# Kernel optimization log

Measured on AMD Instinct MI355X. Metric: run time of the kernel, lower is better.

Reference implementation:

```python
import jax, jax.numpy as jnp
import numpy as np


def setup_inputs() -> dict:
    key = jax.random.key(0)
    kq, kk, kv = jax.random.split(key, 3)
    B, S, D = 4, 4096, 64
    return {
        "q": jax.random.normal(kq, (B, S, D), dtype=jnp.float32),
        "k": jax.random.normal(kk, (B, S, D), dtype=jnp.float32),
        "v": jax.random.normal(kv, (B, S, D), dtype=jnp.float32),
    }


def reference(q, k, v):
    B, S, D = q.shape
    scale = 1.0 / jnp.sqrt(jnp.asarray(D, dtype=q.dtype))
    # (B, S, S) full score matrix, as in the naive torch implementation
    scores = jnp.einsum("bqd,bkd->bqk", q, k) * scale
    causal_mask = jnp.tril(jnp.ones((S, S), dtype=bool))  # True = keep
    scores = jnp.where(causal_mask, scores, -jnp.inf)
    attn = jax.nn.softmax(scores, axis=-1)
    return jnp.einsum("bqk,bkd->bqd", attn, v)
```

## Files before the change

### kernel.cpp

```cpp
#include <hip/hip_runtime.h>
#include <hip/hip_bf16.h>

typedef __bf16 bf16x8 __attribute__((ext_vector_type(8)));
typedef __bf16 bf16x4 __attribute__((ext_vector_type(4)));
typedef float  floatx4 __attribute__((ext_vector_type(4)));

#define SD 4096
#define DH 64
#define NB 4

__device__ __forceinline__ float exp2fast(float x) { return __builtin_amdgcn_exp2f(x); }

__device__ __forceinline__ unsigned pack_bf16_2(float a, float b) {
    union { __bf16 h[2]; unsigned u; } cvt;
    cvt.h[0] = (__bf16)a; cvt.h[1] = (__bf16)b;
    return cvt.u;
}

__device__ __forceinline__ void sync_all() {
    asm volatile("s_waitcnt vmcnt(0) lgkmcnt(0)\n\ts_barrier" ::: "memory");
}

__device__ __forceinline__ void load_lds16(const void* g, void* l) {
    __builtin_amdgcn_global_load_lds(
        (const __attribute__((address_space(1))) unsigned int*)g,
        (__attribute__((address_space(3))) unsigned int*)l, 16, 0, 0);
}

__device__ __forceinline__ int swz8(int g) {
    int row = g >> 3, ch = g & 7;
    return row * 64 + ((ch ^ (row & 7)) << 3);
}

__global__ __launch_bounds__(256) void prep_kernel(const float* __restrict__ k,
                                                   const float* __restrict__ v,
                                                   __bf16* __restrict__ kbs,
                                                   __bf16* __restrict__ vts) {
    __shared__ __bf16 tile[64][72];
    const int bid = blockIdx.x;
    const int tid = threadIdx.x;
    const long base = (long)bid * 4096;

    {
        const float* src = k + base + tid * 16;
        float4 f0 = *(const float4*)(src);
        float4 f1 = *(const float4*)(src + 4);
        float4 f2 = *(const float4*)(src + 8);
        float4 f3 = *(const float4*)(src + 12);
        bf16x8 c0, c1;
        c0[0]=(__bf16)f0.x; c0[1]=(__bf16)f0.y; c0[2]=(__bf16)f0.z; c0[3]=(__bf16)f0.w;
        c0[4]=(__bf16)f1.x; c0[5]=(__bf16)f1.y; c0[6]=(__bf16)f1.z; c0[7]=(__bf16)f1.w;
        c1[0]=(__bf16)f2.x; c1[1]=(__bf16)f2.y; c1[2]=(__bf16)f2.z; c1[3]=(__bf16)f2.w;
        c1[4]=(__bf16)f3.x; c1[5]=(__bf16)f3.y; c1[6]=(__bf16)f3.z; c1[7]=(__bf16)f3.w;
        __bf16* dst = kbs + base;
        *(bf16x8*)(dst + swz8(tid * 2))     = c0;
        *(bf16x8*)(dst + swz8(tid * 2 + 1)) = c1;
    }
    {
        int r = tid >> 2, ds0 = (tid & 3) * 16;
#pragma unroll
        for (int i = 0; i < 4; ++i) {
            float4 f = *(const float4*)(v + base + r * 64 + ds0 + i * 4);
            tile[ds0 + i*4 + 0][r] = (__bf16)f.x;
            tile[ds0 + i*4 + 1][r] = (__bf16)f.y;
            tile[ds0 + i*4 + 2][r] = (__bf16)f.z;
            tile[ds0 + i*4 + 3][r] = (__bf16)f.w;
        }
    }
    __syncthreads();
    {
        __bf16* dst = vts + base;
#pragma unroll
        for (int h = 0; h < 2; ++h) {
            int qc = tid * 2 + h;
            int d = qc >> 3, c8 = (qc & 7) * 8;
            bf16x8 o;
#pragma unroll
            for (int i = 0; i < 8; ++i) {
                int col = c8 + i;
                int key = ((col >> 5) * 2 + ((col >> 2) & 1)) * 16
                        + ((col >> 3) & 3) * 4 + (col & 3);
                o[i] = tile[d][key];
            }
            *(bf16x8*)(dst + swz8(qc)) = o;
        }
    }
}

__global__ __launch_bounds__(256, 4) void fa_kernel(const float* __restrict__ q,
                                                    const __bf16* __restrict__ kbs,
                                                    const __bf16* __restrict__ vts,
                                                    __bf16* __restrict__ opart,
                                                    float* __restrict__ lpart) {
    __shared__ __bf16 smem[2][8192];

    const int tid  = threadIdx.x;
    const int wave = tid >> 6;
    const int lane = tid & 63;
    const int c    = lane & 15;
    const int quad = lane >> 4;
    const int bid   = blockIdx.x;
    const int batch = bid & 3;
    const int pr    = (bid >> 2) & 31;
    const int qr    = bid >> 7;
    const float sc = 0.125f * 1.4426950408889634f;

    const long offB = (long)batch * SD * DH;

    const int sw   = c & 7;
    const int off0 = ((quad ^ sw) << 3);
    const int off1 = (((quad + 4) ^ sw) << 3);
    const int rowc = c * 64;

    const long tileB = (long)batch * 64;

    auto stage = [&](int kt, int bufi) {
        const char* gsrc = (wave < 2)
            ? (const char*)(kbs + (tileB + kt) * 4096) + wave * 4096
            : (const char*)(vts + (tileB + kt) * 4096) + (wave - 2) * 4096;
        char* ldst = (char*)(&smem[bufi][0]) + wave * 4096;
#pragma unroll
        for (int i = 0; i < 4; ++i)
            load_lds16(gsrc + i * 1024 + lane * 16, ldst + i * 1024);
    };

#pragma unroll 1
    for (int ph = 0; ph < 2; ++ph) {
        const int T = ph ? 63 - pr : pr;
        const int myq = T * 64 + wave * 16;
        const int qrow = myq + c;

        bf16x8 qf0, qf1;
        {
            const float* qp = q + offB + (long)(myq + c) * DH + quad * 8;
            float4 f0 = *(const float4*)(qp);
            float4 f1 = *(const float4*)(qp + 4);
            float4 f2 = *(const float4*)(qp + 32);
            float4 f3 = *(const float4*)(qp + 36);
            qf0[0]=(__bf16)(f0.x*sc); qf0[1]=(__bf16)(f0.y*sc); qf0[2]=(__bf16)(f0.z*sc); qf0[3]=(__bf16)(f0.w*sc);
            qf0[4]=(__bf16)(f1.x*sc); qf0[5]=(__bf16)(f1.y*sc); qf0[6]=(__bf16)(f1.z*sc); qf0[7]=(__bf16)(f1.w*sc);
            qf1[0]=(__bf16)(f2.x*sc); qf1[1]=(__bf16)(f2.y*sc); qf1[2]=(__bf16)(f2.z*sc); qf1[3]=(__bf16)(f2.w*sc);
            qf1[4]=(__bf16)(f3.x*sc); qf1[5]=(__bf16)(f3.y*sc); qf1[6]=(__bf16)(f3.z*sc); qf1[7]=(__bf16)(f3.w*sc);
        }

        floatx4 o0 = {0.f,0.f,0.f,0.f}, o1 = o0, o2 = o0, o3 = o0;
        float l = 0.0f;

        const int n = (T >= qr) ? ((T - qr) >> 3) + 1 : 0;

        sync_all();
        if (n > 0) stage(qr, 0);

#pragma unroll 1
        for (int j = 0; j < n; ++j) {
            const int kt = qr + 8 * j;
            sync_all();
            if (j + 1 < n) stage(kt + 8, (j + 1) & 1);

            const int kbase = kt * 64;
            if (kbase > myq + 15) continue;

            const __bf16* kbuf = &smem[j & 1][0];
            const __bf16* vbuf = kbuf + 4096;
            floatx4 sa[4];
#pragma unroll
            for (int t = 0; t < 4; ++t) {
                bf16x8 ka  = *(const bf16x8*)(kbuf + t * 1024 + rowc + off0);
                bf16x8 kb2 = *(const bf16x8*)(kbuf + t * 1024 + rowc + off1);
                floatx4 a = {0.f,0.f,0.f,0.f};
                a = __builtin_amdgcn_mfma_f32_16x16x32_bf16(ka,  qf0, a, 0, 0, 0);
                a = __builtin_amdgcn_mfma_f32_16x16x32_bf16(kb2, qf1, a, 0, 0, 0);
                sa[t] = a;
            }
            float pe[16];
            if (kbase + 63 > myq) {
#pragma unroll
                for (int t = 0; t < 4; ++t)
#pragma unroll
                    for (int r = 0; r < 4; ++r) {
                        int key = kbase + t*16 + quad*4 + r;
                        pe[t*4+r] = (key <= qrow) ? exp2fast(sa[t][r]) : 0.0f;
                    }
            } else {
#pragma unroll
                for (int t = 0; t < 4; ++t)
#pragma unroll
                    for (int r = 0; r < 4; ++r) pe[t*4+r] = exp2fast(sa[t][r]);
            }
            {
                float s8[8], s4v[4];
#pragma unroll
                for (int i = 0; i < 8; ++i) s8[i] = pe[i] + pe[i+8];
#pragma unroll
                for (int i = 0; i < 4; ++i) s4v[i] = s8[i] + s8[i+4];
                l += (s4v[0] + s4v[2]) + (s4v[1] + s4v[3]);
            }
#pragma unroll
            for (int s = 0; s < 2; ++s) {
                union { unsigned u[4]; bf16x8 f; } bp;
#pragma unroll
                for (int jj = 0; jj < 4; ++jj)
                    bp.u[jj] = pack_bf16_2(pe[8*s + 2*jj], pe[8*s + 2*jj + 1]);
                const int offs = s ? off1 : off0;
                bf16x8 v0 = *(const bf16x8*)(vbuf + 0*1024 + rowc + offs);
                bf16x8 v1 = *(const bf16x8*)(vbuf + 1*1024 + rowc + offs);
                bf16x8 v2 = *(const bf16x8*)(vbuf + 2*1024 + rowc + offs);
                bf16x8 v3 = *(const bf16x8*)(vbuf + 3*1024 + rowc + offs);
                o0 = __builtin_amdgcn_mfma_f32_16x16x32_bf16(v0, bp.f, o0, 0, 0, 0);
                o1 = __builtin_amdgcn_mfma_f32_16x16x32_bf16(v1, bp.f, o1, 0, 0, 0);
                o2 = __builtin_amdgcn_mfma_f32_16x16x32_bf16(v2, bp.f, o2, 0, 0, 0);
                o3 = __builtin_amdgcn_mfma_f32_16x16x32_bf16(v3, bp.f, o3, 0, 0, 0);
            }
        }

        l += __shfl_xor(l, 16);
        l += __shfl_xor(l, 32);

        __bf16* ob = opart + ((long)qr * NB + batch) * (long)(SD * DH) + (long)myq * DH;
        {
            floatx4 ov[4] = {o0, o1, o2, o3};
#pragma unroll
            for (int dt = 0; dt < 4; ++dt) {
                uint2 sO;
                sO.x = pack_bf16_2(ov[dt][0], ov[dt][1]);
                sO.y = pack_bf16_2(ov[dt][2], ov[dt][3]);
                *(uint2*)(ob + c * DH + dt*16 + quad*4) = sO;
            }
        }
        if (quad == 0)
            lpart[((long)qr * NB + batch) * SD + myq + c] = l;
    }
}

__global__ __launch_bounds__(256) void combine_kernel(const __bf16* __restrict__ opart,
                                                      const float* __restrict__ lpart,
                                                      float* __restrict__ out) {
    const long t    = (long)blockIdx.x * 256 + threadIdx.x;
    const long base = t * 4;
    const long qq   = base >> 6;
    float n0 = 0.f, n1 = 0.f, n2 = 0.f, n3 = 0.f, den = 0.f;
#pragma unroll
    for (int qr = 0; qr < 8; ++qr) {
        bf16x4 p = *(const bf16x4*)(opart + ((long)qr << 20) + base);
        n0 += (float)p[0]; n1 += (float)p[1]; n2 += (float)p[2]; n3 += (float)p[3];
        den += lpart[((long)qr << 14) + qq];
    }
    float inv = 1.0f / den;
    float4 o; o.x = n0 * inv; o.y = n1 * inv; o.z = n2 * inv; o.w = n3 * inv;
    *(float4*)(out + base) = o;
}

extern "C" void kernel_launch(void* const* d_in, const int* in_sizes, int n_in,
                              void* d_out, int out_size, void* d_ws, size_t ws_size,
                              hipStream_t stream) {
    const float* q = (const float*)d_in[0];
    const float* k = (const float*)d_in[1];
    const float* v = (const float*)d_in[2];
    float* out = (float*)d_out;
    __bf16* kbs   = (__bf16*)d_ws;
    __bf16* vts   = (__bf16*)((char*)d_ws + (2u << 20));
    __bf16* opart = (__bf16*)((char*)d_ws + (4u << 20));
    float*  lpart = (float*)((char*)d_ws + (20u << 20));
    prep_kernel<<<dim3(256), dim3(256), 0, stream>>>(k, v, kbs, vts);
    fa_kernel<<<dim3(1024), dim3(256), 0, stream>>>(q, kbs, vts, opart, lpart);
    combine_kernel<<<dim3(1024), dim3(256), 0, stream>>>(opart, lpart, out);
}
```

Baseline: 91.42 us.

## Fuse split-K combine into attention kernel via last-block atomic counter

Removes the separate combine kernel launch. Each fa_kernel block increments a per-(pair,batch) atomic counter after writing its partials, and the eighth block to finish reduces the partial outputs and denominators and writes the final rows. The counter is zeroed in prep_kernel. This saves a launch and lets the reduction overlap with blocks still computing, at the cost of threadfences, an atomic, and a serialized tail done by a single block per group.

```diff
diff --git a/kernel.cpp b/kernel.cpp
--- a/kernel.cpp
+++ b/kernel.cpp
@@ -35,11 +35,14 @@
 __global__ __launch_bounds__(256) void prep_kernel(const float* __restrict__ k,
                                                    const float* __restrict__ v,
                                                    __bf16* __restrict__ kbs,
-                                                   __bf16* __restrict__ vts) {
+                                                   __bf16* __restrict__ vts,
+                                                   int* __restrict__ cnt) {
     __shared__ __bf16 tile[64][72];
     const int bid = blockIdx.x;
     const int tid = threadIdx.x;
     const long base = (long)bid * 4096;
+
+    if (bid == 0 && tid < 128) cnt[tid] = 0;
 
     {
         const float* src = k + base + tid * 16;
@@ -91,8 +94,11 @@
                                                     const __bf16* __restrict__ kbs,
                                                     const __bf16* __restrict__ vts,
                                                     __bf16* __restrict__ opart,
-                                                    float* __restrict__ lpart) {
+                                                    float* __restrict__ lpart,
+                                                    int* __restrict__ cnt,
+                                                    float* __restrict__ out) {
     __shared__ __bf16 smem[2][8192];
+    __shared__ int slast;
 
     const int tid  = threadIdx.x;
     const int wave = tid >> 6;
@@ -230,24 +236,35 @@
         if (quad == 0)
             lpart[((long)qr * NB + batch) * SD + myq + c] = l;
     }
-}
-
-__global__ __launch_bounds__(256) void combine_kernel(const __bf16* __restrict__ opart,
-                                                      const float* __restrict__ lpart,
-                                                      float* __restrict__ out) {
-    const long t    = (long)blockIdx.x * 256 + threadIdx.x;
-    const long base = t * 4;
-    const long qq   = base >> 6;
-    float n0 = 0.f, n1 = 0.f, n2 = 0.f, n3 = 0.f, den = 0.f;
-#pragma unroll
-    for (int qr = 0; qr < 8; ++qr) {
-        bf16x4 p = *(const bf16x4*)(opart + ((long)qr << 20) + base);
-        n0 += (float)p[0]; n1 += (float)p[1]; n2 += (float)p[2]; n3 += (float)p[3];
-        den += lpart[((long)qr << 14) + qq];
-    }
-    float inv = 1.0f / den;
-    float4 o; o.x = n0 * inv; o.y = n1 * inv; o.z = n2 * inv; o.w = n3 * inv;
-    *(float4*)(out + base) = o;
+
+    __threadfence();
+    if (tid == 0) {
+        int old = atomicAdd(&cnt[pr * NB + batch], 1);
+        slast = (old == 7);
+    }
+    __syncthreads();
+    if (!slast) return;
+    __threadfence();
+
+#pragma unroll 1
+    for (int i = 0; i < 8; ++i) {
+        int oid = tid + 256 * i;
+        int row = oid >> 4;
+        int d4  = (oid & 15) * 4;
+        int qq  = (row < 64) ? pr * 64 + row : (63 - pr) * 64 + (row - 64);
+        const long pbase = (long)qq * DH + d4;
+        float n0 = 0.f, n1 = 0.f, n2 = 0.f, n3 = 0.f, den = 0.f;
+#pragma unroll
+        for (int s = 0; s < 8; ++s) {
+            const long po = ((long)s * NB + batch) * (long)(SD * DH) + pbase;
+            bf16x4 p = *(const bf16x4*)(opart + po);
+            n0 += (float)p[0]; n1 += (float)p[1]; n2 += (float)p[2]; n3 += (float)p[3];
+            den += lpart[((long)s * NB + batch) * SD + qq];
+        }
+        float inv = 1.0f / den;
+        float4 o; o.x = n0 * inv; o.y = n1 * inv; o.z = n2 * inv; o.w = n3 * inv;
+        *(float4*)(out + offB + (long)qq * DH + d4) = o;
+    }
 }
 
 extern "C" void kernel_launch(void* const* d_in, const int* in_sizes, int n_in,
@@ -261,7 +278,7 @@
     __bf16* vts   = (__bf16*)((char*)d_ws + (2u << 20));
     __bf16* opart = (__bf16*)((char*)d_ws + (4u << 20));
     float*  lpart = (float*)((char*)d_ws + (20u << 20));
-    prep_kernel<<<dim3(256), dim3(256), 0, stream>>>(k, v, kbs, vts);
-    fa_kernel<<<dim3(1024), dim3(256), 0, stream>>>(q, kbs, vts, opart, lpart);
-    combine_kernel<<<dim3(1024), dim3(256), 0, stream>>>(opart, lpart, out);
-}
+    int*    cnt   = (int*)((char*)d_ws + (21u << 20));
+    prep_kernel<<<dim3(256), dim3(256), 0, stream>>>(k, v, kbs, vts, cnt);
+    fa_kernel<<<dim3(1024), dim3(256), 0, stream>>>(q, kbs, vts, opart, lpart, cnt, out);
+}
```

Measured after the change: 214.9 us. 2.35x slower.
